# Kernel tuning notes

Measured on AMD Instinct MI355X. Metric: run time of the kernel, lower is better.

## Reference

```python
import jax, jax.numpy as jnp
import numpy as np

H = 32          # num attention heads
KVH = 8         # num kv heads
D = 64          # head dim
HID = 2048      # hidden size
MAXB = 1024     # max_bias_length
BASE = 10000.0  # rope theta


def _rope(x, pos):
    # x: (B, S, h, D), pos: (S,) -- GPT-NeoX half-split rotary
    half = D // 2
    inv_freq = 1.0 / (BASE ** (jnp.arange(0, D, 2, dtype=jnp.float32) / D))  # (half,)
    ang = pos[:, None].astype(jnp.float32) * inv_freq                         # (S, half)
    cos = jnp.cos(ang)[None, :, None, :]
    sin = jnp.sin(ang)[None, :, None, :]
    x1, x2 = x[..., :half], x[..., half:]
    return jnp.concatenate([x1 * cos - x2 * sin, x2 * cos + x1 * sin], axis=-1)


def setup_inputs() -> dict:
    key = jax.random.key(0)
    ks = jax.random.split(key, 7)
    B, S = 2, 1024
    hidden_states = jax.random.normal(ks[0], (B, S, HID), dtype=jnp.float32)
    attention_mask = jnp.broadcast_to(
        jnp.tril(jnp.ones((S, S), dtype=jnp.int32))[None, None], (B, 1, S, S))
    # weights stored as (in, out): y = x @ W  (same math as torch Linear)
    Wq = jax.random.normal(ks[1], (HID, H * D), dtype=jnp.float32) * 0.02
    Wk = jax.random.normal(ks[2], (HID, KVH * D), dtype=jnp.float32) * 0.02
    Wv = jax.random.normal(ks[3], (HID, KVH * D), dtype=jnp.float32) * 0.02
    Wo = jax.random.normal(ks[4], (H * D, HID), dtype=jnp.float32) * 0.02
    bias_diag = jax.random.normal(ks[5], (H, MAXB), dtype=jnp.float32) * 0.001
    softmax_offset = jnp.zeros((H,), dtype=jnp.float32)
    return {"hidden_states": hidden_states, "attention_mask": attention_mask,
            "Wq": Wq, "Wk": Wk, "Wv": Wv, "Wo": Wo,
            "bias_diag": bias_diag, "softmax_offset": softmax_offset}


def reference(hidden_states, attention_mask, Wq, Wk, Wv, Wo, bias_diag, softmax_offset):
    B, S, _ = hidden_states.shape
    scaling = D ** (-0.5)
    pos = jnp.arange(S)

    q = (hidden_states @ Wq).reshape(B, S, H, D)
    k = (hidden_states @ Wk).reshape(B, S, KVH, D)
    v = (hidden_states @ Wv).reshape(B, S, KVH, D)

    q = _rope(q, pos)
    k = _rope(k, pos)

    # (B, H, S, D); repeat_kv via repeat on head axis
    q = q.transpose(0, 2, 1, 3)
    k = jnp.repeat(k.transpose(0, 2, 1, 3), H // KVH, axis=1)
    v = jnp.repeat(v.transpose(0, 2, 1, 3), H // KVH, axis=1)

    scores = jnp.einsum('bhqd,bhkd->bhqk', q, k) * scaling

    # learnable diagonal relative-position bias
    rel = pos[:, None] - pos[None, :]                     # (S, S)
    valid = ((rel >= 0) & (rel < MAXB)).astype(scores.dtype)
    idx = jnp.clip(rel, 0, MAXB - 1)
    bias = bias_diag[:, idx] * valid                      # (H, S, S)
    scores = scores + bias[None]

    scores = jnp.where(attention_mask[:, :, :, :S] == 0, -jnp.inf, scores)

    weights = jax.nn.softmax(scores.astype(jnp.float32), axis=-1)

    # adaptive offset subtraction + relu
    offset = jnp.abs(softmax_offset + 1.0)[None, :, None, None]
    num_visible = (pos + 1).astype(jnp.float32)[None, None, :, None]  # along query dim
    weights = jax.nn.relu(weights - offset / num_visible)

    attn_out = jnp.einsum('bhqk,bhkd->bhqd', weights.astype(v.dtype), v)
    attn_out = attn_out.transpose(0, 2, 1, 3).reshape(B, S, H * D)
    return attn_out @ Wo
```

## Files before the change

kernel.cpp:

```cpp
#include <hip/hip_runtime.h>
#include <cstdint>
#include <cstddef>

#define BB   2
#define SS   1024
#define HID  2048
#define HH   32
#define KVHH 8
#define DD   64
#define NQKV 3072
#define QKW  2560

typedef __attribute__((ext_vector_type(8))) short bf16x8;
typedef __attribute__((ext_vector_type(4))) float f32x4;
typedef __attribute__((ext_vector_type(4))) unsigned int u32x4;

__device__ __forceinline__ unsigned short f2bf(float f) {
    unsigned int u = __float_as_uint(f);
    unsigned int r = (u + 0x7fffu + ((u >> 16) & 1u)) >> 16;
    return (unsigned short)r;
}

__device__ __forceinline__ void g2l16(const unsigned short* g, unsigned short* l) {
    __builtin_amdgcn_global_load_lds(
        (__attribute__((address_space(1))) void*)(unsigned short*)g,
        (__attribute__((address_space(3))) void*)l,
        16, 0, 0);
}

__global__ __launch_bounds__(256) void prep(
    const float* __restrict__ hidden,
    const float* __restrict__ Wq, const float* __restrict__ Wk,
    const float* __restrict__ Wv, const float* __restrict__ Wo,
    unsigned short* __restrict__ hidden_bf,
    unsigned short* __restrict__ WqkvT,
    unsigned short* __restrict__ WoT)
{
    const int z   = blockIdx.z;
    const int tid = threadIdx.x;

    if (z == 4) {
        int r0 = blockIdx.y * 64, c0 = blockIdx.x * 64;
        #pragma unroll
        for (int p = 0; p < 4; ++p) {
            int f = tid + p * 256;
            int row = r0 + (f >> 4), c4 = c0 + (f & 15) * 4;
            float4 v = *(const float4*)&hidden[(size_t)row * 2048 + c4];
            ushort4 o;
            o.x = f2bf(v.x); o.y = f2bf(v.y); o.z = f2bf(v.z); o.w = f2bf(v.w);
            *(ushort4*)&hidden_bf[(size_t)row * 2048 + c4] = o;
        }
        return;
    }

    const float* W;
    unsigned short* Wt;
    int N;
    if (z == 0)      { W = Wq; Wt = WqkvT;                        N = 2048; }
    else if (z == 1) { W = Wk; Wt = WqkvT + (size_t)2048 * 2048;  N = 512;  }
    else if (z == 2) { W = Wv; Wt = WqkvT + (size_t)2560 * 2048;  N = 512;  }
    else             { W = Wo; Wt = WoT;                          N = 2048; }
    if (blockIdx.x * 64 >= N) return;

    __shared__ float t[64][68];
    const int n0 = blockIdx.x * 64, k0 = blockIdx.y * 64;
    #pragma unroll
    for (int p = 0; p < 4; ++p) {
        int f = tid + p * 256;
        int row = f >> 4, c4 = (f & 15) * 4;
        float4 v = *(const float4*)&W[(size_t)(k0 + row) * N + n0 + c4];
        t[row][c4 + 0] = v.x; t[row][c4 + 1] = v.y;
        t[row][c4 + 2] = v.z; t[row][c4 + 3] = v.w;
    }
    __syncthreads();
    #pragma unroll
    for (int p = 0; p < 4; ++p) {
        int f = tid + p * 256;
        int nrow = f >> 4, kc4 = (f & 15) * 4;
        ushort4 o;
        o.x = f2bf(t[kc4 + 0][nrow]);
        o.y = f2bf(t[kc4 + 1][nrow]);
        o.z = f2bf(t[kc4 + 2][nrow]);
        o.w = f2bf(t[kc4 + 3][nrow]);
        *(ushort4*)&Wt[(size_t)(n0 + nrow) * 2048 + k0 + kc4] = o;
    }
}

__global__ __launch_bounds__(256) void gemm_qkv_fused(
    const unsigned short* __restrict__ A,
    const unsigned short* __restrict__ Bt,
    unsigned short* __restrict__ qk_bf,
    unsigned short* __restrict__ v_t)
{
    __shared__ __align__(16) char smem[49152];
    float* Ctf = (float*)smem;

    const int tid  = threadIdx.x;
    const int lane = tid & 63;
    const int wave = tid >> 6;
    const int quad = lane >> 4;
    const int l15  = lane & 15;
    const int wm = (wave >> 1) * 64, wn = (wave & 1) * 32;
    const int m0 = blockIdx.y * 128, n0 = blockIdx.x * 64;
    const int K = 2048;

    f32x4 acc[4][2] = {};

#define STAGE_Q(k0s, buf) do {                                                \
    unsigned short* Ad = (unsigned short*)(smem + (buf) * 24576);             \
    unsigned short* Bd = (unsigned short*)(smem + (buf) * 24576 + 16384);     \
    _Pragma("unroll")                                                         \
    for (int p = 0; p < 4; ++p) {                                             \
        int ci = tid + p * 256;                                               \
        int row_ = ci >> 3, sc_ = (ci & 7) ^ (row_ & 7);                      \
        g2l16(&A[(size_t)(m0 + row_) * K + (k0s) + sc_ * 8], Ad + ci * 8);    \
    }                                                                         \
    _Pragma("unroll")                                                         \
    for (int p = 0; p < 2; ++p) {                                             \
        int ci = tid + p * 256;                                               \
        int row_ = ci >> 3, sc_ = (ci & 7) ^ (row_ & 7);                      \
        g2l16(&Bt[(size_t)(n0 + row_) * K + (k0s) + sc_ * 8], Bd + ci * 8);   \
    } } while (0)

    STAGE_Q(0, 0);
    __syncthreads();
    int cur = 0;
    for (int k0 = 0; k0 < K; k0 += 64) {
        if (k0 + 64 < K) STAGE_Q(k0 + 64, cur ^ 1);
        const short* Ab = (const short*)(smem + cur * 24576);
        const short* Bb = (const short*)(smem + cur * 24576 + 16384);

        #pragma unroll
        for (int s = 0; s < 2; ++s) {
            bf16x8 af[4], bfr[2];
            #pragma unroll
            for (int i = 0; i < 4; ++i) {
                int row = wm + i * 16 + l15;
                af[i] = *(const bf16x8*)(Ab + row * 64 +
                        ((((s << 2) | quad) ^ (row & 7)) * 8));
            }
            #pragma unroll
            for (int j = 0; j < 2; ++j) {
                int row = wn + j * 16 + l15;
                bfr[j] = *(const bf16x8*)(Bb + row * 64 +
                        ((((s << 2) | quad) ^ (row & 7)) * 8));
            }
            #pragma unroll
            for (int i = 0; i < 4; ++i)
                #pragma unroll
                for (int j = 0; j < 2; ++j)
                    acc[i][j] = __builtin_amdgcn_mfma_f32_16x16x32_bf16(
                        af[i], bfr[j], acc[i][j], 0, 0, 0);
        }
        __syncthreads();
        cur ^= 1;
    }

    #pragma unroll
    for (int i = 0; i < 4; ++i)
        #pragma unroll
        for (int j = 0; j < 2; ++j)
            #pragma unroll
            for (int rg = 0; rg < 4; ++rg)
                Ctf[(wm + i * 16 + quad * 4 + rg) * 65 + wn + j * 16 + l15]
                    = acc[i][j][rg];
    __syncthreads();

    const int bx = blockIdx.x;
    const int b  = m0 >> 10;
    const int s0 = m0 & 1023;

    if (bx < 40) {
        const int hc = bx * 64;
        const float scale = (bx < 32) ? 0.125f : 1.0f;
        #pragma unroll
        for (int p = 0; p < 4; ++p) {
            int idx = tid + p * 256;
            int row = idx >> 3, t0 = (idx & 7) * 4;
            int s = s0 + row;
            ushort4 o1, o2;
            #pragma unroll
            for (int k = 0; k < 4; ++k) {
                int t = t0 + k;
                float x1 = Ctf[row * 65 + t];
                float x2 = Ctf[row * 65 + t + 32];
                float inv = __expf(-(float)t * 0.28782313662425572f);
                float ang = (float)s * inv;
                float c  = __cosf(ang);
                float sn = __sinf(ang);
                ((unsigned short*)&o1)[k] = f2bf((x1 * c - x2 * sn) * scale);
                ((unsigned short*)&o2)[k] = f2bf((x2 * c + x1 * sn) * scale);
            }
            unsigned short* dst = qk_bf + (size_t)(m0 + row) * QKW + hc;
            *(ushort4*)&dst[t0]      = o1;
            *(ushort4*)&dst[t0 + 32] = o2;
        }
    } else {
        const int vb = b * 512 + (bx - 40) * 64;
        #pragma unroll
        for (int p = 0; p < 8; ++p) {
            int idx = tid + p * 256;
            int c = idx >> 5, srow = (idx & 31) * 4;
            ushort4 o;
            #pragma unroll
            for (int k = 0; k < 4; ++k)
                ((unsigned short*)&o)[k] = f2bf(Ctf[(srow + k) * 65 + c]);
            *(ushort4*)&v_t[(size_t)(vb + c) * 1024 + s0 + srow] = o;
        }
    }
#undef STAGE_Q
}

__global__ __launch_bounds__(256) void gemm_bf16_bt(
    const unsigned short* __restrict__ A,
    const unsigned short* __restrict__ Bt,
    float* __restrict__ C, int M, int N, int K)
{
    __shared__ __align__(16) char smem[49152];

    const int tid  = threadIdx.x;
    const int lane = tid & 63;
    const int wave = tid >> 6;
    const int quad = lane >> 4;
    const int l15  = lane & 15;
    const int wm = (wave >> 1) * 64, wn = (wave & 1) * 32;
    const int m0 = blockIdx.y * 128, n0 = blockIdx.x * 64;

    f32x4 acc[4][2] = {};

#define STAGE_O(k0s, buf) do {                                                \
    unsigned short* Ad = (unsigned short*)(smem + (buf) * 24576);             \
    unsigned short* Bd = (unsigned short*)(smem + (buf) * 24576 + 16384);     \
    _Pragma("unroll")                                                         \
    for (int p = 0; p < 4; ++p) {                                             \
        int ci = tid + p * 256;                                               \
        int row_ = ci >> 3, sc_ = (ci & 7) ^ (row_ & 7);                      \
        g2l16(&A[(size_t)(m0 + row_) * K + (k0s) + sc_ * 8], Ad + ci * 8);    \
    }                                                                         \
    _Pragma("unroll")                                                         \
    for (int p = 0; p < 2; ++p) {                                             \
        int ci = tid + p * 256;                                               \
        int row_ = ci >> 3, sc_ = (ci & 7) ^ (row_ & 7);                      \
        g2l16(&Bt[(size_t)(n0 + row_) * K + (k0s) + sc_ * 8], Bd + ci * 8);   \
    } } while (0)

    STAGE_O(0, 0);
    __syncthreads();
    int cur = 0;
    for (int k0 = 0; k0 < K; k0 += 64) {
        if (k0 + 64 < K) STAGE_O(k0 + 64, cur ^ 1);
        const short* Ab = (const short*)(smem + cur * 24576);
        const short* Bb = (const short*)(smem + cur * 24576 + 16384);

        #pragma unroll
        for (int s = 0; s < 2; ++s) {
            bf16x8 af[4], bfr[2];
            #pragma unroll
            for (int i = 0; i < 4; ++i) {
                int row = wm + i * 16 + l15;
                af[i] = *(const bf16x8*)(Ab + row * 64 +
                        ((((s << 2) | quad) ^ (row & 7)) * 8));
            }
            #pragma unroll
            for (int j = 0; j < 2; ++j) {
                int row = wn + j * 16 + l15;
                bfr[j] = *(const bf16x8*)(Bb + row * 64 +
                        ((((s << 2) | quad) ^ (row & 7)) * 8));
            }
            #pragma unroll
            for (int i = 0; i < 4; ++i)
                #pragma unroll
                for (int j = 0; j < 2; ++j)
                    acc[i][j] = __builtin_amdgcn_mfma_f32_16x16x32_bf16(
                        af[i], bfr[j], acc[i][j], 0, 0, 0);
        }
        __syncthreads();
        cur ^= 1;
    }

    #pragma unroll
    for (int i = 0; i < 4; ++i) {
        int grow = m0 + wm + i * 16 + quad * 4;
        #pragma unroll
        for (int j = 0; j < 2; ++j) {
            int gcol = n0 + wn + j * 16 + l15;
            #pragma unroll
            for (int rg = 0; rg < 4; ++rg)
                C[(size_t)(grow + rg) * N + gcol] = acc[i][j][rg];
        }
    }
#undef STAGE_O
}

__global__ __launch_bounds__(512, 4) void attn_mfma(
    const unsigned short* __restrict__ qk_bf,
    const unsigned short* __restrict__ v_t,
    const float* __restrict__ bias_diag,
    const float* __restrict__ soff,
    unsigned short* __restrict__ AO)
{
    const int id = (int)blockIdx.x;
    const int h  = id & 31;
    const int b  = (id >> 5) & 1;
    const int pi = id >> 6;
    const int kh = h >> 2;
    const int tid  = threadIdx.x;
    const int lane = tid & 63;
    const int wave = tid >> 6;
    const int grp  = wave >> 2;
    const int w4   = wave & 3;
    const int gt   = tid & 255;
    const int quad = lane >> 4;
    const int l15  = lane & 15;

    __shared__ short Ks[2][2][4096];
    __shared__ short Vs[2][2][4096];
    __shared__ float bd_s[1024];
    __shared__ float red[2][64];

    for (int i = tid; i < 1024; i += 512) bd_s[i] = bias_diag[h * 1024 + i];

    const unsigned short* Kg = qk_bf + (size_t)(b * SS) * QKW + 2048 + kh * 64;
    const unsigned short* Vg = v_t + (size_t)(b * 512 + kh * 64) * SS;

    short* KsG = &Ks[grp][0][0];
    short* VsG = &Vs[grp][0][0];
    float* Fred = (float*)&Ks[1][0][0];

#define STAGE_K(j, buf) do {                                                  \
    _Pragma("unroll")                                                         \
    for (int p = 0; p < 2; ++p) {                                             \
        int ci = gt + p * 256;                                                \
        int row_ = ci >> 3;                                                   \
        int sc_  = (ci & 7) ^ (row_ & 7);                                     \
        g2l16(Kg + (size_t)((j) * 64 + row_) * QKW + sc_ * 8,                 \
              (unsigned short*)(KsG + (buf) * 4096 + ci * 8));                \
    } } while (0)

#define STAGE_V(j, buf) do {                                                  \
    _Pragma("unroll")                                                         \
    for (int p = 0; p < 2; ++p) {                                             \
        int ci = gt + p * 256;                                                \
        int row_ = ci >> 3;                                                   \
        int sc_  = (ci & 7) ^ (row_ & 7);                                     \
        g2l16(Vg + (size_t)row_ * SS + (j) * 64 + sc_ * 8,                    \
              (unsigned short*)(VsG + (buf) * 4096 + ci * 8));                \
    } } while (0)

    #pragma unroll 1
    for (int half = 0; half < 2; ++half) {
        const int qt = half ? pi : 15 - pi;
        const int q0 = qt * 64;
        const int nI = (qt + 2) >> 1;
        const int qrow = q0 + w4 * 16 + l15;

        const unsigned short* Qg =
            qk_bf + (size_t)(b * SS + q0 + w4 * 16) * QKW + h * 64;
        bf16x8 qf0 = *(const bf16x8*)(Qg + (size_t)l15 * QKW + quad * 8);
        bf16x8 qf1 = *(const bf16x8*)(Qg + (size_t)l15 * QKW + 32 + quad * 8);

        float lpa[4] = {0.f, 0.f, 0.f, 0.f};
        if (grp <= qt) STAGE_K(grp, 0);
        __syncthreads();
        int cur = 0;
        for (int i = 0; i < nI; ++i) {
            const int j = 2 * i + grp;
            if (j + 2 <= qt) STAGE_K(j + 2, cur ^ 1);
            if (j <= qt) {
                const short* Kb = KsG + cur * 4096;
                const bool diag = (j == qt);
                f32x4 acc[4] = {};
                #pragma unroll
                for (int nb = 0; nb < 4; ++nb) {
                    if (diag && nb > w4) continue;
                    int row = nb * 16 + l15, sw = row & 7;
                    bf16x8 a0 = *(const bf16x8*)(Kb + row * 64 + ((quad ^ sw) * 8));
                    bf16x8 a1 = *(const bf16x8*)(Kb + row * 64 + (((quad + 4) ^ sw) * 8));
                    acc[nb] = __builtin_amdgcn_mfma_f32_16x16x32_bf16(a0, qf0, acc[nb], 0, 0, 0);
                    acc[nb] = __builtin_amdgcn_mfma_f32_16x16x32_bf16(a1, qf1, acc[nb], 0, 0, 0);
                }
                if (!diag) {
                    #pragma unroll
                    for (int nb = 0; nb < 4; ++nb) {
                        int rel0 = qrow - (j * 64 + nb * 16 + quad * 4);
                        #pragma unroll
                        for (int r = 0; r < 4; ++r)
                            lpa[r] += __expf(acc[nb][r] + bd_s[rel0 - r]);
                    }
                } else {
                    #pragma unroll
                    for (int nb = 0; nb < 4; ++nb) {
                        if (nb > w4) continue;
                        #pragma unroll
                        for (int r = 0; r < 4; ++r) {
                            int rel = qrow - (j * 64 + nb * 16 + quad * 4 + r);
                            if (rel >= 0) lpa[r] += __expf(acc[nb][r] + bd_s[rel]);
                        }
                    }
                }
            }
            __syncthreads();
            cur ^= 1;
        }

        float lp = (lpa[0] + lpa[1]) + (lpa[2] + lpa[3]);
        lp += __shfl_xor(lp, 16, 64);
        lp += __shfl_xor(lp, 32, 64);
        if (quad == 0) red[grp][w4 * 16 + l15] = lp;
        __syncthreads();
        lp = red[0][w4 * 16 + l15] + red[1][w4 * 16 + l15];
        const float invl = 1.f / lp;
        const float cl   = fabsf(soff[h] + 1.f) / (float)(qrow + 1) * lp;

        f32x4 oacc[4] = {};
        if (grp <= qt) { STAGE_K(grp, 0); STAGE_V(grp, 0); }
        __syncthreads();
        cur = 0;
        for (int i = 0; i < nI; ++i) {
            const int j = 2 * i + grp;
            if (j + 2 <= qt) { STAGE_K(j + 2, cur ^ 1); STAGE_V(j + 2, cur ^ 1); }
            if (j <= qt) {
                const short* Kb = KsG + cur * 4096;
                const short* Vb = VsG + cur * 4096;
                const bool diag = (j == qt);

                f32x4 acc[4] = {};
                #pragma unroll
                for (int nb = 0; nb < 4; ++nb) {
                    if (diag && nb > w4) continue;
                    int row = nb * 16 + l15, sw = row & 7;
                    bf16x8 a0 = *(const bf16x8*)(Kb + row * 64 + ((quad ^ sw) * 8));
                    bf16x8 a1 = *(const bf16x8*)(Kb + row * 64 + (((quad + 4) ^ sw) * 8));
                    acc[nb] = __builtin_amdgcn_mfma_f32_16x16x32_bf16(a0, qf0, acc[nb], 0, 0, 0);
                    acc[nb] = __builtin_amdgcn_mfma_f32_16x16x32_bf16(a1, qf1, acc[nb], 0, 0, 0);
                }

                unsigned int pk[4][2];
                if (!diag) {
                    #pragma unroll
                    for (int nb = 0; nb < 4; ++nb) {
                        float w[4];
                        int rel0 = qrow - (j * 64 + nb * 16 + quad * 4);
                        #pragma unroll
                        for (int r = 0; r < 4; ++r)
                            w[r] = fmaxf(__expf(acc[nb][r] + bd_s[rel0 - r]) - cl, 0.f);
                        asm("v_cvt_pk_bf16_f32 %0, %1, %2" : "=v"(pk[nb][0]) : "v"(w[0]), "v"(w[1]));
                        asm("v_cvt_pk_bf16_f32 %0, %1, %2" : "=v"(pk[nb][1]) : "v"(w[2]), "v"(w[3]));
                    }
                } else {
                    #pragma unroll
                    for (int nb = 0; nb < 4; ++nb) {
                        float w[4];
                        #pragma unroll
                        for (int r = 0; r < 4; ++r) {
                            int rel = qrow - (j * 64 + nb * 16 + quad * 4 + r);
                            float e = 0.f;
                            if (rel >= 0)
                                e = fmaxf(__expf(acc[nb][r] + bd_s[rel]) - cl, 0.f);
                            w[r] = e;
                        }
                        asm("v_cvt_pk_bf16_f32 %0, %1, %2" : "=v"(pk[nb][0]) : "v"(w[0]), "v"(w[1]));
                        asm("v_cvt_pk_bf16_f32 %0, %1, %2" : "=v"(pk[nb][1]) : "v"(w[2]), "v"(w[3]));
                    }
                }
                unsigned int ppk[4][2];
                #pragma unroll
                for (int nb = 0; nb < 4; ++nb) {
                    ppk[nb][0] = __shfl_xor(pk[nb][0], 16, 64);
                    ppk[nb][1] = __shfl_xor(pk[nb][1], 16, 64);
                }

                const bool oddq = quad & 1;
                const int  cv   = ((quad & 1) << 1) | (quad >> 1);
                #pragma unroll
                for (int s = 0; s < 2; ++s) {
                    if (diag && s == 1 && w4 < 2) continue;
                    unsigned int w0 = oddq ? ppk[2 * s + 1][0] : pk[2 * s][0];
                    unsigned int w1 = oddq ? ppk[2 * s + 1][1] : pk[2 * s][1];
                    unsigned int w2 = oddq ? pk[2 * s + 1][0]  : ppk[2 * s][0];
                    unsigned int w3 = oddq ? pk[2 * s + 1][1]  : ppk[2 * s][1];
                    u32x4 t; t[0] = w0; t[1] = w1; t[2] = w2; t[3] = w3;
                    bf16x8 pf = __builtin_bit_cast(bf16x8, t);
                    #pragma unroll
                    for (int nd = 0; nd < 4; ++nd) {
                        int rowv = nd * 16 + l15, swv = rowv & 7;
                        bf16x8 vf = *(const bf16x8*)(Vb + rowv * 64 + (((cv + 4 * s) ^ swv) * 8));
                        oacc[nd] = __builtin_amdgcn_mfma_f32_16x16x32_bf16(pf, vf, oacc[nd], 0, 0, 0);
                    }
                }
            }
            __syncthreads();
            cur ^= 1;
        }

        if (grp == 1) {
            #pragma unroll
            for (int nd = 0; nd < 4; ++nd)
                #pragma unroll
                for (int r = 0; r < 4; ++r)
                    Fred[(w4 * 16 + quad * 4 + r) * 64 + nd * 16 + l15] = oacc[nd][r];
        }
        __syncthreads();
        if (grp == 0) {
            float invl_r[4];
            #pragma unroll
            for (int r = 0; r < 4; ++r)
                invl_r[r] = __shfl(invl, quad * 4 + r, 64);
            unsigned short* aop =
                AO + (size_t)(b * SS + q0 + w4 * 16 + quad * 4) * 2048 + h * 64 + l15;
            #pragma unroll
            for (int nd = 0; nd < 4; ++nd)
                #pragma unroll
                for (int r = 0; r < 4; ++r) {
                    float o = (oacc[nd][r] +
                               Fred[(w4 * 16 + quad * 4 + r) * 64 + nd * 16 + l15])
                              * invl_r[r];
                    aop[(size_t)r * 2048 + nd * 16] = f2bf(o);
                }
        }
        __syncthreads();
    }
#undef STAGE_K
#undef STAGE_V
}

extern "C" void kernel_launch(void* const* d_in, const int* in_sizes, int n_in,
                              void* d_out, int out_size, void* d_ws, size_t ws_size,
                              hipStream_t stream)
{
    const float* hidden    = (const float*)d_in[0];
    const float* Wq        = (const float*)d_in[2];
    const float* Wk        = (const float*)d_in[3];
    const float* Wv        = (const float*)d_in[4];
    const float* Wo        = (const float*)d_in[5];
    const float* bias_diag = (const float*)d_in[6];
    const float* soff      = (const float*)d_in[7];
    float* out = (float*)d_out;

    char* wsb = (char*)d_ws;
    unsigned short* hidden_bf = (unsigned short*)wsb;
    unsigned short* WqkvT     = (unsigned short*)(wsb + (size_t)8388608);
    unsigned short* AO_bf     = (unsigned short*)(wsb + (size_t)12582912);
    unsigned short* WoT       = (unsigned short*)(wsb + (size_t)20971520);
    unsigned short* qk_bf     = (unsigned short*)(wsb + (size_t)29360128);
    unsigned short* v_t       = (unsigned short*)(wsb + (size_t)29360128 + (size_t)2048 * 2560 * 2);

    prep<<<dim3(32, 32, 5), dim3(256), 0, stream>>>(
        hidden, Wq, Wk, Wv, Wo, hidden_bf, WqkvT, WoT);

    gemm_qkv_fused<<<dim3(48, 16), dim3(256), 0, stream>>>(
        hidden_bf, WqkvT, qk_bf, v_t);

    attn_mfma<<<dim3(512), dim3(512), 0, stream>>>(
        qk_bf, v_t, bias_diag, soff, AO_bf);

    gemm_bf16_bt<<<dim3(2048 / 64, 2048 / 128), dim3(256), 0, stream>>>(
        AO_bf, WoT, out, 2048, 2048, 2048);
}
```

Baseline: 203.2 us.

## Restructure attention to 128-row query tiles, swizzle GEMM grids, use exp2

The attention kernel now has each 8-wave block own a single 128-row query tile, with all waves sharing one K/V stream instead of two wave groups splitting the key blocks. That removes the cross-group reduction through shared memory and the two-pass half loop. The block-to-tile mapping reverses tile order for the first half of blocks to balance causal work. Softmax uses the raw v_exp_f32 (exp2) instruction, with log2(e) folded into the Q scale and the bias table. Both GEMMs remap block indices with a swizzle for better L2 locality, and the attention launch-bounds occupancy hint is dropped.

```diff
diff --git a/kernel.cpp b/kernel.cpp
--- a/kernel.cpp
+++ b/kernel.cpp
@@ -19,6 +19,10 @@
     unsigned int u = __float_as_uint(f);
     unsigned int r = (u + 0x7fffu + ((u >> 16) & 1u)) >> 16;
     return (unsigned short)r;
+}
+
+__device__ __forceinline__ float ex2(float x) {
+    float r; asm("v_exp_f32 %0, %1" : "=v"(r) : "v"(x)); return r;
 }
 
 __device__ __forceinline__ void g2l16(const unsigned short* g, unsigned short* l) {
@@ -101,7 +105,12 @@
     const int quad = lane >> 4;
     const int l15  = lane & 15;
     const int wm = (wave >> 1) * 64, wn = (wave & 1) * 32;
-    const int m0 = blockIdx.y * 128, n0 = blockIdx.x * 64;
+
+    const int lin = (int)blockIdx.x + (int)blockIdx.y * 48;
+    const int swz = (lin & 7) * 96 + (lin >> 3);
+    const int bx  = swz % 48, by = swz / 48;
+
+    const int m0 = by * 128, n0 = bx * 64;
     const int K = 2048;
 
     f32x4 acc[4][2] = {};
@@ -166,13 +175,12 @@
                     = acc[i][j][rg];
     __syncthreads();
 
-    const int bx = blockIdx.x;
     const int b  = m0 >> 10;
     const int s0 = m0 & 1023;
 
     if (bx < 40) {
         const int hc = bx * 64;
-        const float scale = (bx < 32) ? 0.125f : 1.0f;
+        const float scale = (bx < 32) ? 0.18033688011112042f : 1.0f;
         #pragma unroll
         for (int p = 0; p < 4; ++p) {
             int idx = tid + p * 256;
@@ -224,7 +232,12 @@
     const int quad = lane >> 4;
     const int l15  = lane & 15;
     const int wm = (wave >> 1) * 64, wn = (wave & 1) * 32;
-    const int m0 = blockIdx.y * 128, n0 = blockIdx.x * 64;
+
+    const int lin = (int)blockIdx.x + (int)blockIdx.y * 32;
+    const int swz = (lin & 7) * 64 + (lin >> 3);
+    const int bx  = swz % 32, by = swz / 32;
+
+    const int m0 = by * 128, n0 = bx * 64;
 
     f32x4 acc[4][2] = {};
 
@@ -292,7 +305,7 @@
 #undef STAGE_O
 }
 
-__global__ __launch_bounds__(512, 4) void attn_mfma(
+__global__ __launch_bounds__(512) void attn_mfma(
     const unsigned short* __restrict__ qk_bf,
     const unsigned short* __restrict__ v_t,
     const float* __restrict__ bias_diag,
@@ -300,226 +313,202 @@
     unsigned short* __restrict__ AO)
 {
     const int id = (int)blockIdx.x;
-    const int h  = id & 31;
-    const int b  = (id >> 5) & 1;
-    const int pi = id >> 6;
+    const int t8 = id & 7;
+    const int qt2 = (id < 256) ? (7 - t8) : t8;
+    const int hb = id >> 3;
+    const int h  = hb & 31;
+    const int b  = hb >> 5;
     const int kh = h >> 2;
     const int tid  = threadIdx.x;
     const int lane = tid & 63;
     const int wave = tid >> 6;
-    const int grp  = wave >> 2;
-    const int w4   = wave & 3;
-    const int gt   = tid & 255;
     const int quad = lane >> 4;
     const int l15  = lane & 15;
-
-    __shared__ short Ks[2][2][4096];
-    __shared__ short Vs[2][2][4096];
+    const int q0   = qt2 * 128;
+    const int J    = 2 * qt2 + 2;
+
+    __shared__ short Ks[2][4096];
+    __shared__ short Vs[2][4096];
     __shared__ float bd_s[1024];
-    __shared__ float red[2][64];
-
-    for (int i = tid; i < 1024; i += 512) bd_s[i] = bias_diag[h * 1024 + i];
+
+    for (int i = tid; i < 1024; i += 512)
+        bd_s[i] = bias_diag[h * 1024 + i] * 1.4426950408889634f;
 
     const unsigned short* Kg = qk_bf + (size_t)(b * SS) * QKW + 2048 + kh * 64;
     const unsigned short* Vg = v_t + (size_t)(b * 512 + kh * 64) * SS;
 
-    short* KsG = &Ks[grp][0][0];
-    short* VsG = &Vs[grp][0][0];
-    float* Fred = (float*)&Ks[1][0][0];
+    const int qrow = q0 + wave * 16 + l15;
+
+    const unsigned short* Qg =
+        qk_bf + (size_t)(b * SS + q0 + wave * 16) * QKW + h * 64;
+    bf16x8 qf0 = *(const bf16x8*)(Qg + (size_t)l15 * QKW + quad * 8);
+    bf16x8 qf1 = *(const bf16x8*)(Qg + (size_t)l15 * QKW + 32 + quad * 8);
 
 #define STAGE_K(j, buf) do {                                                  \
-    _Pragma("unroll")                                                         \
-    for (int p = 0; p < 2; ++p) {                                             \
-        int ci = gt + p * 256;                                                \
-        int row_ = ci >> 3;                                                   \
-        int sc_  = (ci & 7) ^ (row_ & 7);                                     \
-        g2l16(Kg + (size_t)((j) * 64 + row_) * QKW + sc_ * 8,                 \
-              (unsigned short*)(KsG + (buf) * 4096 + ci * 8));                \
-    } } while (0)
+    int ci = tid;                                                             \
+    int row_ = ci >> 3, sc_ = (ci & 7) ^ (row_ & 7);                          \
+    g2l16(Kg + (size_t)((j) * 64 + row_) * QKW + sc_ * 8,                     \
+          (unsigned short*)&Ks[buf][ci * 8]);                                 \
+} while (0)
 
 #define STAGE_V(j, buf) do {                                                  \
-    _Pragma("unroll")                                                         \
-    for (int p = 0; p < 2; ++p) {                                             \
-        int ci = gt + p * 256;                                                \
-        int row_ = ci >> 3;                                                   \
-        int sc_  = (ci & 7) ^ (row_ & 7);                                     \
-        g2l16(Vg + (size_t)row_ * SS + (j) * 64 + sc_ * 8,                    \
-              (unsigned short*)(VsG + (buf) * 4096 + ci * 8));                \
-    } } while (0)
-
-    #pragma unroll 1
-    for (int half = 0; half < 2; ++half) {
-        const int qt = half ? pi : 15 - pi;
-        const int q0 = qt * 64;
-        const int nI = (qt + 2) >> 1;
-        const int qrow = q0 + w4 * 16 + l15;
-
-        const unsigned short* Qg =
-            qk_bf + (size_t)(b * SS + q0 + w4 * 16) * QKW + h * 64;
-        bf16x8 qf0 = *(const bf16x8*)(Qg + (size_t)l15 * QKW + quad * 8);
-        bf16x8 qf1 = *(const bf16x8*)(Qg + (size_t)l15 * QKW + 32 + quad * 8);
-
-        float lpa[4] = {0.f, 0.f, 0.f, 0.f};
-        if (grp <= qt) STAGE_K(grp, 0);
-        __syncthreads();
-        int cur = 0;
-        for (int i = 0; i < nI; ++i) {
-            const int j = 2 * i + grp;
-            if (j + 2 <= qt) STAGE_K(j + 2, cur ^ 1);
-            if (j <= qt) {
-                const short* Kb = KsG + cur * 4096;
-                const bool diag = (j == qt);
-                f32x4 acc[4] = {};
+    int ci = tid;                                                             \
+    int row_ = ci >> 3, sc_ = (ci & 7) ^ (row_ & 7);                          \
+    g2l16(Vg + (size_t)row_ * SS + (j) * 64 + sc_ * 8,                        \
+          (unsigned short*)&Vs[buf][ci * 8]);                                 \
+} while (0)
+
+    float lpa[4] = {0.f, 0.f, 0.f, 0.f};
+    STAGE_K(0, 0);
+    __syncthreads();
+    int cur = 0;
+    for (int j = 0; j < J; ++j) {
+        if (j + 1 < J) STAGE_K(j + 1, cur ^ 1);
+        const int dj = j - 2 * qt2;
+        const bool full = (dj < 0) || (dj == 0 && wave >= 4);
+        const bool dead = (dj == 1 && wave < 4);
+        const int  wd   = (dj == 0) ? wave : wave - 4;
+        const bool diag = !full && !dead;
+
+        if (!dead) {
+            const short* Kb = Ks[cur];
+            f32x4 acc[4] = {};
+            #pragma unroll
+            for (int nb = 0; nb < 4; ++nb) {
+                if (diag && nb > wd) continue;
+                int row = nb * 16 + l15, sw = row & 7;
+                bf16x8 a0 = *(const bf16x8*)(Kb + row * 64 + ((quad ^ sw) * 8));
+                bf16x8 a1 = *(const bf16x8*)(Kb + row * 64 + (((quad + 4) ^ sw) * 8));
+                acc[nb] = __builtin_amdgcn_mfma_f32_16x16x32_bf16(a0, qf0, acc[nb], 0, 0, 0);
+                acc[nb] = __builtin_amdgcn_mfma_f32_16x16x32_bf16(a1, qf1, acc[nb], 0, 0, 0);
+            }
+            if (full) {
                 #pragma unroll
                 for (int nb = 0; nb < 4; ++nb) {
-                    if (diag && nb > w4) continue;
-                    int row = nb * 16 + l15, sw = row & 7;
-                    bf16x8 a0 = *(const bf16x8*)(Kb + row * 64 + ((quad ^ sw) * 8));
-                    bf16x8 a1 = *(const bf16x8*)(Kb + row * 64 + (((quad + 4) ^ sw) * 8));
-                    acc[nb] = __builtin_amdgcn_mfma_f32_16x16x32_bf16(a0, qf0, acc[nb], 0, 0, 0);
-                    acc[nb] = __builtin_amdgcn_mfma_f32_16x16x32_bf16(a1, qf1, acc[nb], 0, 0, 0);
+                    int rel0 = qrow - (j * 64 + nb * 16 + quad * 4);
+                    #pragma unroll
+                    for (int r = 0; r < 4; ++r)
+                        lpa[r] += ex2(acc[nb][r] + bd_s[rel0 - r]);
                 }
-                if (!diag) {
+            } else {
+                #pragma unroll
+                for (int nb = 0; nb < 4; ++nb) {
+                    if (nb > wd) continue;
                     #pragma unroll
-                    for (int nb = 0; nb < 4; ++nb) {
-                        int rel0 = qrow - (j * 64 + nb * 16 + quad * 4);
-                        #pragma unroll
-                        for (int r = 0; r < 4; ++r)
-                            lpa[r] += __expf(acc[nb][r] + bd_s[rel0 - r]);
-                    }
-                } else {
-                    #pragma unroll
-                    for (int nb = 0; nb < 4; ++nb) {
-                        if (nb > w4) continue;
-                        #pragma unroll
-                        for (int r = 0; r < 4; ++r) {
-                            int rel = qrow - (j * 64 + nb * 16 + quad * 4 + r);
-                            if (rel >= 0) lpa[r] += __expf(acc[nb][r] + bd_s[rel]);
-                        }
+                    for (int r = 0; r < 4; ++r) {
+                        int rel = qrow - (j * 64 + nb * 16 + quad * 4 + r);
+                        if (rel >= 0) lpa[r] += ex2(acc[nb][r] + bd_s[rel]);
                     }
                 }
             }
-            __syncthreads();
-            cur ^= 1;
-        }
-
-        float lp = (lpa[0] + lpa[1]) + (lpa[2] + lpa[3]);
-        lp += __shfl_xor(lp, 16, 64);
-        lp += __shfl_xor(lp, 32, 64);
-        if (quad == 0) red[grp][w4 * 16 + l15] = lp;
+        }
         __syncthreads();
-        lp = red[0][w4 * 16 + l15] + red[1][w4 * 16 + l15];
-        const float invl = 1.f / lp;
-        const float cl   = fabsf(soff[h] + 1.f) / (float)(qrow + 1) * lp;
-
-        f32x4 oacc[4] = {};
-        if (grp <= qt) { STAGE_K(grp, 0); STAGE_V(grp, 0); }
+        cur ^= 1;
+    }
+
+    float lp = (lpa[0] + lpa[1]) + (lpa[2] + lpa[3]);
+    lp += __shfl_xor(lp, 16, 64);
+    lp += __shfl_xor(lp, 32, 64);
+    const float invl = 1.f / lp;
+    const float cl   = fabsf(soff[h] + 1.f) / (float)(qrow + 1) * lp;
+
+    f32x4 oacc[4] = {};
+    STAGE_K(0, 0);
+    STAGE_V(0, 0);
+    __syncthreads();
+    cur = 0;
+    for (int j = 0; j < J; ++j) {
+        if (j + 1 < J) { STAGE_K(j + 1, cur ^ 1); STAGE_V(j + 1, cur ^ 1); }
+        const int dj = j - 2 * qt2;
+        const bool full = (dj < 0) || (dj == 0 && wave >= 4);
+        const bool dead = (dj == 1 && wave < 4);
+        const int  wd   = (dj == 0) ? wave : wave - 4;
+        const bool diag = !full && !dead;
+
+        if (!dead) {
+            const short* Kb = Ks[cur];
+            const short* Vb = Vs[cur];
+
+            f32x4 acc[4] = {};
+            #pragma unroll
+            for (int nb = 0; nb < 4; ++nb) {
+                if (diag && nb > wd) continue;
+                int row = nb * 16 + l15, sw = row & 7;
+                bf16x8 a0 = *(const bf16x8*)(Kb + row * 64 + ((quad ^ sw) * 8));
+                bf16x8 a1 = *(const bf16x8*)(Kb + row * 64 + (((quad + 4) ^ sw) * 8));
+                acc[nb] = __builtin_amdgcn_mfma_f32_16x16x32_bf16(a0, qf0, acc[nb], 0, 0, 0);
+                acc[nb] = __builtin_amdgcn_mfma_f32_16x16x32_bf16(a1, qf1, acc[nb], 0, 0, 0);
+            }
+
+            unsigned int pk[4][2];
+            if (full) {
+                #pragma unroll
+                for (int nb = 0; nb < 4; ++nb) {
+                    float w[4];
+                    int rel0 = qrow - (j * 64 + nb * 16 + quad * 4);
+                    #pragma unroll
+                    for (int r = 0; r < 4; ++r)
+                        w[r] = fmaxf(ex2(acc[nb][r] + bd_s[rel0 - r]) - cl, 0.f);
+                    asm("v_cvt_pk_bf16_f32 %0, %1, %2" : "=v"(pk[nb][0]) : "v"(w[0]), "v"(w[1]));
+                    asm("v_cvt_pk_bf16_f32 %0, %1, %2" : "=v"(pk[nb][1]) : "v"(w[2]), "v"(w[3]));
+                }
+            } else {
+                #pragma unroll
+                for (int nb = 0; nb < 4; ++nb) {
+                    float w[4];
+                    #pragma unroll
+                    for (int r = 0; r < 4; ++r) {
+                        int rel = qrow - (j * 64 + nb * 16 + quad * 4 + r);
+                        float e = 0.f;
+                        if (rel >= 0)
+                            e = fmaxf(ex2(acc[nb][r] + bd_s[rel]) - cl, 0.f);
+                        w[r] = e;
+                    }
+                    asm("v_cvt_pk_bf16_f32 %0, %1, %2" : "=v"(pk[nb][0]) : "v"(w[0]), "v"(w[1]));
+                    asm("v_cvt_pk_bf16_f32 %0, %1, %2" : "=v"(pk[nb][1]) : "v"(w[2]), "v"(w[3]));
+                }
+            }
+            unsigned int ppk[4][2];
+            #pragma unroll
+            for (int nb = 0; nb < 4; ++nb) {
+                ppk[nb][0] = __shfl_xor(pk[nb][0], 16, 64);
+                ppk[nb][1] = __shfl_xor(pk[nb][1], 16, 64);
+            }
+
+            const bool oddq = quad & 1;
+            const int  cv   = ((quad & 1) << 1) | (quad >> 1);
+            #pragma unroll
+            for (int s = 0; s < 2; ++s) {
+                if (diag && s == 1 && wd < 2) continue;
+                unsigned int w0 = oddq ? ppk[2 * s + 1][0] : pk[2 * s][0];
+                unsigned int w1 = oddq ? ppk[2 * s + 1][1] : pk[2 * s][1];
+                unsigned int w2 = oddq ? pk[2 * s + 1][0]  : ppk[2 * s][0];
+                unsigned int w3 = oddq ? pk[2 * s + 1][1]  : ppk[2 * s][1];
+                u32x4 t; t[0] = w0; t[1] = w1; t[2] = w2; t[3] = w3;
+                bf16x8 pf = __builtin_bit_cast(bf16x8, t);
+                #pragma unroll
+                for (int nd = 0; nd < 4; ++nd) {
+                    int rowv = nd * 16 + l15, swv = rowv & 7;
+                    bf16x8 vf = *(const bf16x8*)(Vb + rowv * 64 + (((cv + 4 * s) ^ swv) * 8));
+                    oacc[nd] = __builtin_amdgcn_mfma_f32_16x16x32_bf16(pf, vf, oacc[nd], 0, 0, 0);
+                }
+            }
+        }
         __syncthreads();
-        cur = 0;
-        for (int i = 0; i < nI; ++i) {
-            const int j = 2 * i + grp;
-            if (j + 2 <= qt) { STAGE_K(j + 2, cur ^ 1); STAGE_V(j + 2, cur ^ 1); }
-            if (j <= qt) {
-                const short* Kb = KsG + cur * 4096;
-                const short* Vb = VsG + cur * 4096;
-                const bool diag = (j == qt);
-
-                f32x4 acc[4] = {};
-                #pragma unroll
-                for (int nb = 0; nb < 4; ++nb) {
-                    if (diag && nb > w4) continue;
-                    int row = nb * 16 + l15, sw = row & 7;
-                    bf16x8 a0 = *(const bf16x8*)(Kb + row * 64 + ((quad ^ sw) * 8));
-                    bf16x8 a1 = *(const bf16x8*)(Kb + row * 64 + (((quad + 4) ^ sw) * 8));
-                    acc[nb] = __builtin_amdgcn_mfma_f32_16x16x32_bf16(a0, qf0, acc[nb], 0, 0, 0);
-                    acc[nb] = __builtin_amdgcn_mfma_f32_16x16x32_bf16(a1, qf1, acc[nb], 0, 0, 0);
-                }
-
-                unsigned int pk[4][2];
-                if (!diag) {
-                    #pragma unroll
-                    for (int nb = 0; nb < 4; ++nb) {
-                        float w[4];
-                        int rel0 = qrow - (j * 64 + nb * 16 + quad * 4);
-                        #pragma unroll
-                        for (int r = 0; r < 4; ++r)
-                            w[r] = fmaxf(__expf(acc[nb][r] + bd_s[rel0 - r]) - cl, 0.f);
-                        asm("v_cvt_pk_bf16_f32 %0, %1, %2" : "=v"(pk[nb][0]) : "v"(w[0]), "v"(w[1]));
-                        asm("v_cvt_pk_bf16_f32 %0, %1, %2" : "=v"(pk[nb][1]) : "v"(w[2]), "v"(w[3]));
-                    }
-                } else {
-                    #pragma unroll
-                    for (int nb = 0; nb < 4; ++nb) {
-                        float w[4];
-                        #pragma unroll
-                        for (int r = 0; r < 4; ++r) {
-                            int rel = qrow - (j * 64 + nb * 16 + quad * 4 + r);
-                            float e = 0.f;
-                            if (rel >= 0)
-                                e = fmaxf(__expf(acc[nb][r] + bd_s[rel]) - cl, 0.f);
-                            w[r] = e;
-                        }
-                        asm("v_cvt_pk_bf16_f32 %0, %1, %2" : "=v"(pk[nb][0]) : "v"(w[0]), "v"(w[1]));
-                        asm("v_cvt_pk_bf16_f32 %0, %1, %2" : "=v"(pk[nb][1]) : "v"(w[2]), "v"(w[3]));
-                    }
-                }
-                unsigned int ppk[4][2];
-                #pragma unroll
-                for (int nb = 0; nb < 4; ++nb) {
-                    ppk[nb][0] = __shfl_xor(pk[nb][0], 16, 64);
-                    ppk[nb][1] = __shfl_xor(pk[nb][1], 16, 64);
-                }
-
-                const bool oddq = quad & 1;
-                const int  cv   = ((quad & 1) << 1) | (quad >> 1);
-                #pragma unroll
-                for (int s = 0; s < 2; ++s) {
-                    if (diag && s == 1 && w4 < 2) continue;
-                    unsigned int w0 = oddq ? ppk[2 * s + 1][0] : pk[2 * s][0];
-                    unsigned int w1 = oddq ? ppk[2 * s + 1][1] : pk[2 * s][1];
-                    unsigned int w2 = oddq ? pk[2 * s + 1][0]  : ppk[2 * s][0];
-                    unsigned int w3 = oddq ? pk[2 * s + 1][1]  : ppk[2 * s][1];
-                    u32x4 t; t[0] = w0; t[1] = w1; t[2] = w2; t[3] = w3;
-                    bf16x8 pf = __builtin_bit_cast(bf16x8, t);
-                    #pragma unroll
-                    for (int nd = 0; nd < 4; ++nd) {
-                        int rowv = nd * 16 + l15, swv = rowv & 7;
-                        bf16x8 vf = *(const bf16x8*)(Vb + rowv * 64 + (((cv + 4 * s) ^ swv) * 8));
-                        oacc[nd] = __builtin_amdgcn_mfma_f32_16x16x32_bf16(pf, vf, oacc[nd], 0, 0, 0);
-                    }
-                }
-            }
-            __syncthreads();
-            cur ^= 1;
-        }
-
-        if (grp == 1) {
-            #pragma unroll
-            for (int nd = 0; nd < 4; ++nd)
-                #pragma unroll
-                for (int r = 0; r < 4; ++r)
-                    Fred[(w4 * 16 + quad * 4 + r) * 64 + nd * 16 + l15] = oacc[nd][r];
-        }
-        __syncthreads();
-        if (grp == 0) {
-            float invl_r[4];
-            #pragma unroll
-            for (int r = 0; r < 4; ++r)
-                invl_r[r] = __shfl(invl, quad * 4 + r, 64);
-            unsigned short* aop =
-                AO + (size_t)(b * SS + q0 + w4 * 16 + quad * 4) * 2048 + h * 64 + l15;
-            #pragma unroll
-            for (int nd = 0; nd < 4; ++nd)
-                #pragma unroll
-                for (int r = 0; r < 4; ++r) {
-                    float o = (oacc[nd][r] +
-                               Fred[(w4 * 16 + quad * 4 + r) * 64 + nd * 16 + l15])
-                              * invl_r[r];
-                    aop[(size_t)r * 2048 + nd * 16] = f2bf(o);
-                }
-        }
-        __syncthreads();
-    }
+        cur ^= 1;
+    }
+
+    float invl_r[4];
+    #pragma unroll
+    for (int r = 0; r < 4; ++r)
+        invl_r[r] = __shfl(invl, quad * 4 + r, 64);
+    unsigned short* aop =
+        AO + (size_t)(b * SS + q0 + wave * 16 + quad * 4) * 2048 + h * 64 + l15;
+    #pragma unroll
+    for (int nd = 0; nd < 4; ++nd)
+        #pragma unroll
+        for (int r = 0; r < 4; ++r)
+            aop[(size_t)r * 2048 + nd * 16] = f2bf(oacc[nd][r] * invl_r[r]);
 #undef STAGE_K
 #undef STAGE_V
 }
```

New measurement: 213.0 us. +4.9%, slower.
